# Optimization experiments

Measured on AMD Instinct MI355X. Metric: run time of the kernel, lower is better.

Reference implementation:

```python
import jax, jax.numpy as jnp
import numpy as np

B, S, D, H = 4, 1024, 2048, 16
HD = D // H
SCALE = float(np.sqrt(HD))


def setup_inputs() -> dict:
    key = jax.random.key(0)
    ks = jax.random.split(key, 11)
    std = 1.0 / np.sqrt(D)
    inp = {
        'q': jax.random.normal(ks[0], (B, S, D), jnp.float32),
        'k': jax.random.normal(ks[1], (B, S, D), jnp.float32),
        'v': jax.random.normal(ks[2], (B, S, D), jnp.float32),
        'wq_w': jax.random.uniform(ks[3], (D, D), jnp.float32, -std, std),
        'wq_b': jax.random.uniform(ks[4], (D,), jnp.float32, -std, std),
        'wk_w': jax.random.uniform(ks[5], (D, D), jnp.float32, -std, std),
        'wk_b': jax.random.uniform(ks[6], (D,), jnp.float32, -std, std),
        'wv_w': jax.random.uniform(ks[7], (D, D), jnp.float32, -std, std),
        'wv_b': jax.random.uniform(ks[8], (D,), jnp.float32, -std, std),
        'wo_w': jax.random.uniform(ks[9], (D, D), jnp.float32, -std, std),
        'wo_b': jax.random.uniform(ks[10], (D,), jnp.float32, -std, std),
    }
    return inp


def reference(q, k, v, wq_w, wq_b, wk_w, wk_b, wv_w, wv_b, wo_w, wo_b):
    # Linear projections (torch Linear: x @ W.T + b), split into heads: [B,H,S,HD]
    Q = (q @ wq_w.T + wq_b).reshape(B, S, H, HD).transpose(0, 2, 1, 3)
    K = (k @ wk_w.T + wk_b).reshape(B, S, H, HD).transpose(0, 2, 1, 3)
    V = (v @ wv_w.T + wv_b).reshape(B, S, H, HD).transpose(0, 2, 1, 3)
    # scaled dot-product attention; mask=None, dropout identity (eval)
    scores = jnp.einsum('bhqd,bhkd->bhqk', Q, K) / SCALE  # [B,H,S,S]
    attn = jax.nn.softmax(scores, axis=-1)
    context = jnp.einsum('bhqk,bhkd->bhqd', attn, V)      # [B,H,S,HD]
    context = context.transpose(0, 2, 1, 3).reshape(B, S, D)
    output = context @ wo_w.T + wo_b
    return output, attn
```

## Files before the change

kernel.cpp:

```cpp
#include <hip/hip_runtime.h>
#include <hip/hip_bf16.h>


typedef __attribute__((ext_vector_type(4)))  float f32x4;
typedef __attribute__((ext_vector_type(16))) float f32x16;
typedef __attribute__((ext_vector_type(8))) short  bf16x8;
typedef __attribute__((ext_vector_type(4))) short  short4v;
typedef __attribute__((ext_vector_type(8))) short  short8v;

__device__ __forceinline__ short f2b(float f) {
  __hip_bfloat16 h = __float2bfloat16(f);
  return __builtin_bit_cast(short, h);
}
__device__ __forceinline__ float b2f(short s) {
  __hip_bfloat16 h = __builtin_bit_cast(__hip_bfloat16, s);
  return __bfloat162float(h);
}

__global__ void cast_bf16(const float* __restrict__ in, __hip_bfloat16* __restrict__ out, size_t n) {
  size_t i0 = ((size_t)blockIdx.x * blockDim.x + threadIdx.x) * 8;
  size_t stride = (size_t)gridDim.x * blockDim.x * 8;
  for (size_t i = i0; i < n; i += stride) {
    float4 a = *(const float4*)(in + i);
    float4 b = *(const float4*)(in + i + 4);
    short8v o;
    o[0] = f2b(a.x); o[1] = f2b(a.y); o[2] = f2b(a.z); o[3] = f2b(a.w);
    o[4] = f2b(b.x); o[5] = f2b(b.y); o[6] = f2b(b.z); o[7] = f2b(b.w);
    *(short8v*)(out + i) = o;
  }
}

__device__ __forceinline__ void gload_lds16(const __hip_bfloat16* g, char* l) {
  __builtin_amdgcn_global_load_lds(
      (const __attribute__((address_space(1))) unsigned int*)g,
      (__attribute__((address_space(3))) unsigned int*)l, 16, 0, 0);
}

template<int MODE>
__global__ __launch_bounds__(256, 2) void gemm_bt(
    const __hip_bfloat16* __restrict__ A,
    const __hip_bfloat16* __restrict__ Bt,
    const float* __restrict__ bias,
    void* __restrict__ outp,
    int M, int N, int K)
{
  __shared__ __align__(16) char As[128 * 64];
  __shared__ __align__(16) char Bs[128 * 64];
  const int tid  = threadIdx.x;
  const int lane = tid & 63, wid = tid >> 6;
  const int l16  = lane & 15, g = lane >> 4;
  const int m0 = blockIdx.y * 128, n0 = blockIdx.x * 128;
  const int wm = (wid >> 1) * 64, wn = (wid & 1) * 64;
  const size_t Kz = (size_t)K;

  f32x4 acc[4][4];
#pragma unroll
  for (int i = 0; i < 4; ++i)
#pragma unroll
    for (int j = 0; j < 4; ++j) acc[i][j] = f32x4{0.f, 0.f, 0.f, 0.f};

  const __hip_bfloat16* ga0 = A  + (size_t)(m0 + wid * 32 + (lane >> 2)) * Kz + (lane & 3) * 8;
  const __hip_bfloat16* gb0 = Bt + (size_t)(n0 + wid * 32 + (lane >> 2)) * Kz + (lane & 3) * 8;
  char* lA0 = As + wid * 2048;
  char* lB0 = Bs + wid * 2048;

  const int nk = K >> 5;
  for (int kt = 0; kt < nk; ++kt) {
    __syncthreads();
    gload_lds16(ga0,            lA0);
    gload_lds16(ga0 + 16 * Kz,  lA0 + 1024);
    gload_lds16(gb0,            lB0);
    gload_lds16(gb0 + 16 * Kz,  lB0 + 1024);
    ga0 += 32; gb0 += 32;
    asm volatile("s_waitcnt vmcnt(0)" ::: "memory");
    __syncthreads();
    bf16x8 a[4], b[4];
#pragma unroll
    for (int mf = 0; mf < 4; ++mf)
      a[mf] = *(const bf16x8*)(As + (wm + mf * 16 + l16) * 64 + g * 16);
#pragma unroll
    for (int nf = 0; nf < 4; ++nf)
      b[nf] = *(const bf16x8*)(Bs + (wn + nf * 16 + l16) * 64 + g * 16);
#pragma unroll
    for (int mf = 0; mf < 4; ++mf)
#pragma unroll
      for (int nf = 0; nf < 4; ++nf)
        acc[mf][nf] = __builtin_amdgcn_mfma_f32_16x16x32_bf16(a[mf], b[nf], acc[mf][nf], 0, 0, 0);
  }

  if (MODE == 2) {
    float* C = (float*)outp;
#pragma unroll
    for (int nf = 0; nf < 4; ++nf) {
      int col = n0 + wn + nf * 16 + l16;
      float bv = bias[col];
#pragma unroll
      for (int mf = 0; mf < 4; ++mf) {
        int row = m0 + wm + mf * 16 + g * 4;
#pragma unroll
        for (int r = 0; r < 4; ++r)
          C[(size_t)(row + r) * N + col] = acc[mf][nf][r] + bv;
      }
    }
  } else if (MODE == 0) {
    __hip_bfloat16* C = (__hip_bfloat16*)outp;
#pragma unroll
    for (int nf = 0; nf < 4; ++nf) {
      int col = n0 + wn + nf * 16 + l16;
      float bv = bias[col];
      int h = col >> 7, hd = col & 127;
#pragma unroll
      for (int mf = 0; mf < 4; ++mf) {
        int row = m0 + wm + mf * 16 + g * 4;
        int bb = row >> 10, s = row & 1023;
        size_t base = (((size_t)bb * 16 + h) * 1024 + s) * 128 + hd;
#pragma unroll
        for (int r = 0; r < 4; ++r)
          C[base + (size_t)r * 128] = __float2bfloat16(acc[mf][nf][r] + bv);
      }
    }
  } else {
    __hip_bfloat16* C = (__hip_bfloat16*)outp;
#pragma unroll
    for (int nf = 0; nf < 4; ++nf) {
      int col = n0 + wn + nf * 16 + l16;
      float bv = bias[col];
      int h = col >> 7, hd = col & 127;
#pragma unroll
      for (int mf = 0; mf < 4; ++mf) {
        int row = m0 + wm + mf * 16 + g * 4;
        int bb = row >> 10, s = row & 1023;
        size_t base = (((size_t)bb * 16 + h) * 128 + hd) * 1024 + s;
        short4v pk;
#pragma unroll
        for (int r = 0; r < 4; ++r) pk[r] = f2b(acc[mf][nf][r] + bv);
        *(short4v*)(C + base) = pk;
      }
    }
  }
}

__global__ __launch_bounds__(512, 4) void attn_kernel(
    const __hip_bfloat16* __restrict__ Qh,
    const __hip_bfloat16* __restrict__ Kh,
    const __hip_bfloat16* __restrict__ Vt,
    float* __restrict__ attn,
    __hip_bfloat16* __restrict__ ctx)
{
  __shared__ __align__(16) char Plds[32 * 2048];
  __shared__ float red[8 * 32];
  __shared__ float invs[32];

  const int tid = threadIdx.x, lane = tid & 63, w = tid >> 6;
  const int l16 = lane & 15, g = lane >> 4;
  const int l31 = lane & 31, kh = lane >> 5;

  const int bid = blockIdx.x;
  const int xcd = bid & 7, j = bid >> 3;
  const int bh  = xcd * 8 + (j >> 5);
  const int q0  = (j & 31) << 5;

  const __hip_bfloat16* Qp = Qh + ((size_t)bh * 1024 + q0) * 128;
  const __hip_bfloat16* Kp = Kh + (size_t)bh * 1024 * 128;
  const __hip_bfloat16* Vp = Vt + (size_t)bh * 128 * 1024;
  float* ap = attn + ((size_t)bh * 1024 + q0) * 1024;

  bf16x8 qb[8];
#pragma unroll
  for (int s = 0; s < 8; ++s)
    qb[s] = *(const bf16x8*)(Qp + (size_t)l31 * 128 + s * 16 + kh * 8);

  const float esc = 0.08838834764831845f;
  float rs = 0.f;

#pragma unroll
  for (int pass = 0; pass < 4; ++pass) {
    const int keybase = pass * 256 + w * 32;
    const __hip_bfloat16* kr = Kp + (size_t)(keybase + l31) * 128 + kh * 8;
    bf16x8 kb[8];
#pragma unroll
    for (int s = 0; s < 8; ++s) kb[s] = *(const bf16x8*)(kr + s * 16);
    f32x16 acc;
#pragma unroll
    for (int i = 0; i < 16; ++i) acc[i] = 0.f;
    __builtin_amdgcn_s_setprio(1);
#pragma unroll
    for (int s = 0; s < 8; ++s)
      acc = __builtin_amdgcn_mfma_f32_32x32x16_bf16(kb[s], qb[s], acc, 0, 0, 0);
    __builtin_amdgcn_s_setprio(0);
#pragma unroll
    for (int grp = 0; grp < 4; ++grp) {
      short4v pk;
#pragma unroll
      for (int jj = 0; jj < 4; ++jj) {
        float e = __expf(acc[grp * 4 + jj] * esc);
        rs += e;
        pk[jj] = f2b(e);
      }
      int key0 = keybase + grp * 8 + kh * 4;
      *(short4v*)(Plds + l31 * 2048 + ((key0 * 2) ^ ((l31 & 7) << 4))) = pk;
    }
  }
  rs += __shfl_xor(rs, 32, 64);
  if (lane < 32) red[w * 32 + l31] = rs;
  __syncthreads();
  if (tid < 32) {
    float t = 0.f;
#pragma unroll
    for (int ww = 0; ww < 8; ++ww) t += red[ww * 32 + tid];
    invs[tid] = 1.0f / t;
  }
  __syncthreads();

  {
    const int row = 4 * w + g;
    const float invr = invs[row];
    const char* rp = Plds + row * 2048;
    const int sw = (row & 7) << 4;
    float* apr = ap + (size_t)row * 1024;
#pragma unroll
    for (int it = 0; it < 16; ++it) {
      int col = it * 64 + l16 * 4;
      short4v pb = *(const short4v*)(rp + ((col * 2) ^ sw));
      f32x4 val;
#pragma unroll
      for (int r = 0; r < 4; ++r) val[r] = b2f(pb[r]) * invr;
      __builtin_nontemporal_store(val, (f32x4*)(apr + col));
    }
  }

  f32x4 acc2[2];
  acc2[0] = f32x4{0.f, 0.f, 0.f, 0.f};
  acc2[1] = f32x4{0.f, 0.f, 0.f, 0.f};
  {
    const char* pr0 = Plds + l16 * 2048;
    const char* pr1 = Plds + (16 + l16) * 2048;
    const int sw = (l16 & 7) << 4;
#pragma unroll 4
    for (int kt = 0; kt < 32; ++kt) {
      int cb = (kt * 64 + g * 16) ^ sw;
      bf16x8 pa0 = *(const bf16x8*)(pr0 + cb);
      bf16x8 pa1 = *(const bf16x8*)(pr1 + cb);
      const __hip_bfloat16* vr = Vp + (size_t)(16 * w + l16) * 1024 + kt * 32 + g * 8;
      bf16x8 vb = *(const bf16x8*)vr;
      __builtin_amdgcn_s_setprio(1);
      acc2[0] = __builtin_amdgcn_mfma_f32_16x16x32_bf16(pa0, vb, acc2[0], 0, 0, 0);
      acc2[1] = __builtin_amdgcn_mfma_f32_16x16x32_bf16(pa1, vb, acc2[1], 0, 0, 0);
      __builtin_amdgcn_s_setprio(0);
    }
  }
  __syncthreads();

  {
    __hip_bfloat16* cs = (__hip_bfloat16*)Plds;
#pragma unroll
    for (int t = 0; t < 2; ++t) {
      f32x4 iv = *(const f32x4*)(invs + t * 16 + g * 4);
#pragma unroll
      for (int r = 0; r < 4; ++r)
        cs[(t * 16 + g * 4 + r) * 128 + 16 * w + l16] = __float2bfloat16(acc2[t][r] * iv[r]);
    }
    __syncthreads();
    const int row = tid >> 4, c8 = (tid & 15) * 8;
    bf16x8 val = *(const bf16x8*)(cs + row * 128 + c8);
    const int bb = bh >> 4, h = bh & 15;
    *(bf16x8*)(ctx + ((size_t)(bb * 1024 + q0 + row)) * 2048 + h * 128 + c8) = val;
  }
}

extern "C" void kernel_launch(void* const* d_in, const int* in_sizes, int n_in,
                              void* d_out, int out_size, void* d_ws, size_t ws_size,
                              hipStream_t stream) {
  const float* q    = (const float*)d_in[0];
  const float* k    = (const float*)d_in[1];
  const float* v    = (const float*)d_in[2];
  const float* wq_w = (const float*)d_in[3];
  const float* wq_b = (const float*)d_in[4];
  const float* wk_w = (const float*)d_in[5];
  const float* wk_b = (const float*)d_in[6];
  const float* wv_w = (const float*)d_in[7];
  const float* wv_b = (const float*)d_in[8];
  const float* wo_w = (const float*)d_in[9];
  const float* wo_b = (const float*)d_in[10];

  const size_t BSD = (size_t)4 * 1024 * 2048;
  const size_t DD  = (size_t)2048 * 2048;

  float* out  = (float*)d_out;
  float* attn = out + BSD;

  __hip_bfloat16* qbf = (__hip_bfloat16*)attn;
  __hip_bfloat16* kbf = qbf + BSD;
  __hip_bfloat16* vbf = kbf + BSD;

  __hip_bfloat16* wqb = (__hip_bfloat16*)d_ws;
  __hip_bfloat16* wkb = wqb + DD;
  __hip_bfloat16* wvb = wkb + DD;
  __hip_bfloat16* wob = wvb + DD;
  __hip_bfloat16* Qh  = wob + DD;
  __hip_bfloat16* Kh  = Qh + BSD;
  __hip_bfloat16* Vt  = Kh + BSD;
  __hip_bfloat16* ctx = Vt + BSD;

  dim3 cb(256);
  cast_bf16<<<2048, cb, 0, stream>>>(q, qbf, BSD);
  cast_bf16<<<2048, cb, 0, stream>>>(k, kbf, BSD);
  cast_bf16<<<2048, cb, 0, stream>>>(v, vbf, BSD);
  cast_bf16<<<2048, cb, 0, stream>>>(wq_w, wqb, DD);
  cast_bf16<<<2048, cb, 0, stream>>>(wk_w, wkb, DD);
  cast_bf16<<<2048, cb, 0, stream>>>(wv_w, wvb, DD);
  cast_bf16<<<2048, cb, 0, stream>>>(wo_w, wob, DD);

  dim3 gg(16, 32), gb(256);
  gemm_bt<0><<<gg, gb, 0, stream>>>(qbf, wqb, wq_b, Qh, 4096, 2048, 2048);
  gemm_bt<0><<<gg, gb, 0, stream>>>(kbf, wkb, wk_b, Kh, 4096, 2048, 2048);
  gemm_bt<1><<<gg, gb, 0, stream>>>(vbf, wvb, wv_b, Vt, 4096, 2048, 2048);

  attn_kernel<<<dim3(2048), dim3(512), 0, stream>>>(Qh, Kh, Vt, attn, ctx);

  gemm_bt<2><<<gg, gb, 0, stream>>>(ctx, wob, wo_b, out, 4096, 2048, 2048);
}
```

Baseline: 411.0 us.

## Fuse cast kernels, batch Q/K GEMMs, and stage GEMM epilogues through LDS

Merges the seven fp32-to-bf16 cast launches into one kernel and runs the Q and K projections as a single grid with a z dimension. The GEMM epilogues now swap the MFMA operand order or stage tiles through padded shared memory, so the head-split Q/K/V outputs and the fp32 output are written with wide coalesced stores instead of scattered 2- or 4-byte writes. This targets launch overhead and uncoalesced epilogue stores. In exchange it enlarges the shared-memory footprint (the new buffer sizes also differ from the 128*64 tiles the hidden load path uses) and adds extra barriers.

New measurement: 379.6 us. 7.6% less time.

```diff
diff --git a/kernel.cpp b/kernel.cpp
--- a/kernel.cpp
+++ b/kernel.cpp
@@ -17,16 +17,35 @@
   return __bfloat162float(h);
 }
 
-__global__ void cast_bf16(const float* __restrict__ in, __hip_bfloat16* __restrict__ out, size_t n) {
-  size_t i0 = ((size_t)blockIdx.x * blockDim.x + threadIdx.x) * 8;
-  size_t stride = (size_t)gridDim.x * blockDim.x * 8;
-  for (size_t i = i0; i < n; i += stride) {
-    float4 a = *(const float4*)(in + i);
-    float4 b = *(const float4*)(in + i + 4);
+__global__ void cast_all(
+    const float* __restrict__ q,  const float* __restrict__ k,  const float* __restrict__ v,
+    const float* __restrict__ w0, const float* __restrict__ w1, const float* __restrict__ w2,
+    const float* __restrict__ w3,
+    __hip_bfloat16* __restrict__ qd, __hip_bfloat16* __restrict__ kd, __hip_bfloat16* __restrict__ vd,
+    __hip_bfloat16* __restrict__ d0, __hip_bfloat16* __restrict__ d1, __hip_bfloat16* __restrict__ d2,
+    __hip_bfloat16* __restrict__ d3)
+{
+  const int c0 = blockIdx.x * blockDim.x + threadIdx.x;
+#pragma unroll
+  for (int it = 0; it < 10; ++it) {
+    int c = c0 + it * 524288;
+    const float* in; __hip_bfloat16* out; size_t off;
+    if (c < 3145728) {
+      int seg = c >> 20; off = (size_t)(c & 1048575) * 8;
+      in  = seg == 0 ? q  : (seg == 1 ? k  : v);
+      out = seg == 0 ? qd : (seg == 1 ? kd : vd);
+    } else {
+      int c2 = c - 3145728;
+      int seg = c2 >> 19; off = (size_t)(c2 & 524287) * 8;
+      in  = seg == 0 ? w0 : (seg == 1 ? w1 : (seg == 2 ? w2 : w3));
+      out = seg == 0 ? d0 : (seg == 1 ? d1 : (seg == 2 ? d2 : d3));
+    }
+    float4 a = *(const float4*)(in + off);
+    float4 b = *(const float4*)(in + off + 4);
     short8v o;
     o[0] = f2b(a.x); o[1] = f2b(a.y); o[2] = f2b(a.z); o[3] = f2b(a.w);
     o[4] = f2b(b.x); o[5] = f2b(b.y); o[6] = f2b(b.z); o[7] = f2b(b.w);
-    *(short8v*)(out + i) = o;
+    *(short8v*)(out + off) = o;
   }
 }
 
@@ -37,15 +56,23 @@
 }
 
 template<int MODE>
-__global__ __launch_bounds__(256, 2) void gemm_bt(
-    const __hip_bfloat16* __restrict__ A,
-    const __hip_bfloat16* __restrict__ Bt,
-    const float* __restrict__ bias,
-    void* __restrict__ outp,
+__global__ __launch_bounds__(256, 2) void gemm_bt2(
+    const __hip_bfloat16* __restrict__ A0, const __hip_bfloat16* __restrict__ A1,
+    const __hip_bfloat16* __restrict__ B0, const __hip_bfloat16* __restrict__ B1,
+    const float* __restrict__ bias0, const float* __restrict__ bias1,
+    void* __restrict__ out0, void* __restrict__ out1,
     int M, int N, int K)
 {
-  __shared__ __align__(16) char As[128 * 64];
-  __shared__ __align__(16) char Bs[128 * 64];
+  __shared__ __align__(16) char smem[MODE == 2 ? 32768 : 34816];
+  char* As = smem;
+  char* Bs = smem + 16384;
+
+  const int z = (MODE == 0) ? blockIdx.z : 0;
+  const __hip_bfloat16* A  = z ? A1 : A0;
+  const __hip_bfloat16* Bt = z ? B1 : B0;
+  const float* bias        = z ? bias1 : bias0;
+  void* outp               = z ? out1 : out0;
+
   const int tid  = threadIdx.x;
   const int lane = tid & 63, wid = tid >> 6;
   const int l16  = lane & 15, g = lane >> 4;
@@ -84,58 +111,80 @@
 #pragma unroll
     for (int mf = 0; mf < 4; ++mf)
 #pragma unroll
-      for (int nf = 0; nf < 4; ++nf)
-        acc[mf][nf] = __builtin_amdgcn_mfma_f32_16x16x32_bf16(a[mf], b[nf], acc[mf][nf], 0, 0, 0);
+      for (int nf = 0; nf < 4; ++nf) {
+        if (MODE == 1)
+          acc[mf][nf] = __builtin_amdgcn_mfma_f32_16x16x32_bf16(a[mf], b[nf], acc[mf][nf], 0, 0, 0);
+        else
+          acc[mf][nf] = __builtin_amdgcn_mfma_f32_16x16x32_bf16(b[nf], a[mf], acc[mf][nf], 0, 0, 0);
+      }
   }
 
   if (MODE == 2) {
     float* C = (float*)outp;
 #pragma unroll
     for (int nf = 0; nf < 4; ++nf) {
-      int col = n0 + wn + nf * 16 + l16;
-      float bv = bias[col];
+      f32x4 bv = *(const f32x4*)(bias + n0 + wn + nf * 16 + g * 4);
 #pragma unroll
       for (int mf = 0; mf < 4; ++mf) {
-        int row = m0 + wm + mf * 16 + g * 4;
-#pragma unroll
-        for (int r = 0; r < 4; ++r)
-          C[(size_t)(row + r) * N + col] = acc[mf][nf][r] + bv;
+        int m = m0 + wm + mf * 16 + l16;
+        int n = n0 + wn + nf * 16 + g * 4;
+        f32x4 o;
+#pragma unroll
+        for (int r = 0; r < 4; ++r) o[r] = acc[mf][nf][r] + bv[r];
+        *(f32x4*)(C + (size_t)m * N + n) = o;
       }
     }
   } else if (MODE == 0) {
+    __syncthreads();
+    char* Cs = smem;
+#pragma unroll
+    for (int nf = 0; nf < 4; ++nf) {
+      f32x4 bv = *(const f32x4*)(bias + n0 + wn + nf * 16 + g * 4);
+#pragma unroll
+      for (int mf = 0; mf < 4; ++mf) {
+        int m  = wm + mf * 16 + l16;
+        int nc = wn + nf * 16 + g * 4;
+        short4v pk;
+#pragma unroll
+        for (int r = 0; r < 4; ++r) pk[r] = f2b(acc[mf][nf][r] + bv[r]);
+        *(short4v*)(Cs + m * 272 + nc * 2) = pk;
+      }
+    }
+    __syncthreads();
     __hip_bfloat16* C = (__hip_bfloat16*)outp;
+    const int h = n0 >> 7, bb = m0 >> 10, sbase = m0 & 1023;
+    const int c8 = (tid & 15) * 8;
+#pragma unroll
+    for (int p = 0; p < 8; ++p) {
+      int row = p * 16 + (tid >> 4);
+      bf16x8 val = *(const bf16x8*)(Cs + row * 272 + c8 * 2);
+      *(bf16x8*)(C + (((size_t)bb * 16 + h) * 1024 + sbase + row) * 128 + c8) = val;
+    }
+  } else {
+    __syncthreads();
+    char* Cs = smem;
 #pragma unroll
     for (int nf = 0; nf < 4; ++nf) {
-      int col = n0 + wn + nf * 16 + l16;
-      float bv = bias[col];
-      int h = col >> 7, hd = col & 127;
+      float bv = bias[n0 + wn + nf * 16 + l16];
 #pragma unroll
       for (int mf = 0; mf < 4; ++mf) {
-        int row = m0 + wm + mf * 16 + g * 4;
-        int bb = row >> 10, s = row & 1023;
-        size_t base = (((size_t)bb * 16 + h) * 1024 + s) * 128 + hd;
-#pragma unroll
-        for (int r = 0; r < 4; ++r)
-          C[base + (size_t)r * 128] = __float2bfloat16(acc[mf][nf][r] + bv);
-      }
-    }
-  } else {
+        int hd = wn + nf * 16 + l16;
+        int s0 = wm + mf * 16 + g * 4;
+        short4v pk;
+#pragma unroll
+        for (int r = 0; r < 4; ++r) pk[r] = f2b(acc[mf][nf][r] + bv);
+        *(short4v*)(Cs + hd * 272 + s0 * 2) = pk;
+      }
+    }
+    __syncthreads();
     __hip_bfloat16* C = (__hip_bfloat16*)outp;
-#pragma unroll
-    for (int nf = 0; nf < 4; ++nf) {
-      int col = n0 + wn + nf * 16 + l16;
-      float bv = bias[col];
-      int h = col >> 7, hd = col & 127;
-#pragma unroll
-      for (int mf = 0; mf < 4; ++mf) {
-        int row = m0 + wm + mf * 16 + g * 4;
-        int bb = row >> 10, s = row & 1023;
-        size_t base = (((size_t)bb * 16 + h) * 128 + hd) * 1024 + s;
-        short4v pk;
-#pragma unroll
-        for (int r = 0; r < 4; ++r) pk[r] = f2b(acc[mf][nf][r] + bv);
-        *(short4v*)(C + base) = pk;
-      }
+    const int h = n0 >> 7, bb = m0 >> 10, sbase = m0 & 1023;
+    const int c8 = (tid & 15) * 8;
+#pragma unroll
+    for (int p = 0; p < 8; ++p) {
+      int hd = p * 16 + (tid >> 4);
+      bf16x8 val = *(const bf16x8*)(Cs + hd * 272 + c8 * 2);
+      *(bf16x8*)(C + (((size_t)bb * 16 + h) * 128 + hd) * 1024 + sbase + c8) = val;
     }
   }
 }
@@ -302,21 +351,17 @@
   __hip_bfloat16* Vt  = Kh + BSD;
   __hip_bfloat16* ctx = Vt + BSD;
 
-  dim3 cb(256);
-  cast_bf16<<<2048, cb, 0, stream>>>(q, qbf, BSD);
-  cast_bf16<<<2048, cb, 0, stream>>>(k, kbf, BSD);
-  cast_bf16<<<2048, cb, 0, stream>>>(v, vbf, BSD);
-  cast_bf16<<<2048, cb, 0, stream>>>(wq_w, wqb, DD);
-  cast_bf16<<<2048, cb, 0, stream>>>(wk_w, wkb, DD);
-  cast_bf16<<<2048, cb, 0, stream>>>(wv_w, wvb, DD);
-  cast_bf16<<<2048, cb, 0, stream>>>(wo_w, wob, DD);
-
-  dim3 gg(16, 32), gb(256);
-  gemm_bt<0><<<gg, gb, 0, stream>>>(qbf, wqb, wq_b, Qh, 4096, 2048, 2048);
-  gemm_bt<0><<<gg, gb, 0, stream>>>(kbf, wkb, wk_b, Kh, 4096, 2048, 2048);
-  gemm_bt<1><<<gg, gb, 0, stream>>>(vbf, wvb, wv_b, Vt, 4096, 2048, 2048);
+  cast_all<<<2048, 256, 0, stream>>>(q, k, v, wq_w, wk_w, wv_w, wo_w,
+                                     qbf, kbf, vbf, wqb, wkb, wvb, wob);
+
+  dim3 gb(256);
+  gemm_bt2<0><<<dim3(16, 32, 2), gb, 0, stream>>>(qbf, kbf, wqb, wkb, wq_b, wk_b,
+                                                  Qh, Kh, 4096, 2048, 2048);
+  gemm_bt2<1><<<dim3(16, 32), gb, 0, stream>>>(vbf, vbf, wvb, wvb, wv_b, wv_b,
+                                               Vt, Vt, 4096, 2048, 2048);
 
   attn_kernel<<<dim3(2048), dim3(512), 0, stream>>>(Qh, Kh, Vt, attn, ctx);
 
-  gemm_bt<2><<<gg, gb, 0, stream>>>(ctx, wob, wo_b, out, 4096, 2048, 2048);
-}
+  gemm_bt2<2><<<dim3(16, 32), gb, 0, stream>>>(ctx, ctx, wob, wob, wo_b, wo_b,
+                                               out, out, 4096, 2048, 2048);
+}
```
